# Kernel optimization log

Hardware: AMD Instinct MI355X
Metric: run time of the kernel (lower is better)

The kernel has to match this reference:

```python
import jax, jax.numpy as jnp
import numpy as np

NU, NI, D, H = 200000, 100000, 128, 128
E = 600000

def _segment_mean(vals, seg_ids, num_segments):
    s = jax.ops.segment_sum(vals, seg_ids, num_segments=num_segments)
    cnt = jax.ops.segment_sum(jnp.ones((vals.shape[0],), vals.dtype), seg_ids, num_segments=num_segments)
    return s / jnp.maximum(cnt, 1.0)[:, None]


def setup_inputs() -> dict:
    key = jax.random.key(0)
    ks = jax.random.split(key, 16)
    sc = 1.0 / np.sqrt(D)
    return {
        'x_user': jax.random.normal(ks[0], (NU, D), jnp.float32),
        'x_item': jax.random.normal(ks[1], (NI, D), jnp.float32),
        'edge_src_ui': jax.random.randint(ks[2], (E,), 0, NU),
        'edge_dst_ui': jax.random.randint(ks[3], (E,), 0, NI),
        'edge_src_iu': jax.random.randint(ks[4], (E,), 0, NI),
        'edge_dst_iu': jax.random.randint(ks[5], (E,), 0, NU),
        'Wl_ui': jax.random.normal(ks[6], (D, H), jnp.float32) * sc,
        'bl_ui': jax.random.normal(ks[7], (H,), jnp.float32) * 0.01,
        'Wr_ui': jax.random.normal(ks[8], (D, H), jnp.float32) * sc,
        'Wl_iu': jax.random.normal(ks[9], (D, H), jnp.float32) * sc,
        'bl_iu': jax.random.normal(ks[10], (H,), jnp.float32) * 0.01,
        'Wr_iu': jax.random.normal(ks[11], (D, H), jnp.float32) * sc,
        'W_user': jax.random.normal(ks[12], (H, H), jnp.float32) * sc,
        'b_user': jax.random.normal(ks[13], (H,), jnp.float32) * 0.01,
        'W_item': jax.random.normal(ks[14], (H, H), jnp.float32) * sc,
        'b_item': jax.random.normal(ks[15], (H,), jnp.float32) * 0.01,
    }


def reference(x_user, x_item, edge_src_ui, edge_dst_ui, edge_src_iu, edge_dst_iu,
              Wl_ui, bl_ui, Wr_ui, Wl_iu, bl_iu, Wr_iu,
              W_user, b_user, W_item, b_item):
    # SAGEConv per edge type: out_dst = mean_aggr(x_src[src]) @ Wl + bl + x_dst @ Wr
    agg_item = _segment_mean(x_user[edge_src_ui], edge_dst_ui, NI)   # [NI, D]
    h_item = agg_item @ Wl_ui + bl_ui + x_item @ Wr_ui               # [NI, H]
    agg_user = _segment_mean(x_item[edge_src_iu], edge_dst_iu, NU)   # [NU, D]
    h_user = agg_user @ Wl_iu + bl_iu + x_user @ Wr_iu               # [NU, H]
    # HeteroConv aggr='sum' is trivial here (one edge type per dst node type).
    out_user = jax.nn.relu(h_user @ W_user + b_user)
    out_item = jax.nn.relu(h_item @ W_item + b_item)
    return jnp.concatenate([out_user, out_item], axis=0)  # [NU+NI, H]
```

## Files before the change

### kernel.cpp

```cpp
#include <hip/hip_runtime.h>

#define NUu 200000
#define NIi 100000
#define EE  600000

#define SCAP 1024

typedef short short8 __attribute__((ext_vector_type(8)));
typedef float floatx4 __attribute__((ext_vector_type(4)));

__device__ __forceinline__ unsigned short f2bf(float f) {
  union { float f; unsigned int u; } v; v.f = f;
  unsigned int r = v.u + 0x7FFFu + ((v.u >> 16) & 1u);
  return (unsigned short)(r >> 16);
}

__global__ __launch_bounds__(128) void fuse_weights(
    const float* __restrict__ Wl_iu, const float* __restrict__ Wr_iu,
    const float* __restrict__ Wl_ui, const float* __restrict__ Wr_ui,
    const float* __restrict__ W_user, const float* __restrict__ W_item,
    unsigned short* __restrict__ Wp_user, unsigned short* __restrict__ Wp_item)
{
  int d = blockIdx.x;
  int m = blockIdx.y;
  int h = threadIdx.x;
  const float* A; const float* W; unsigned short* dst; int koff;
  switch (m) {
    case 0:  A = Wl_iu; W = W_user; dst = Wp_user; koff = 0;   break;
    case 1:  A = Wr_iu; W = W_user; dst = Wp_user; koff = 128; break;
    case 2:  A = Wl_ui; W = W_item; dst = Wp_item; koff = 0;   break;
    default: A = Wr_ui; W = W_item; dst = Wp_item; koff = 128; break;
  }
  float acc = 0.f;
  for (int k = 0; k < 128; ++k) acc += A[d * 128 + k] * W[k * 128 + h];
  int kg = koff + d;
  int ks = kg >> 5, quad = (kg >> 3) & 3, j = kg & 7;
  int nt = h >> 4, nlo = h & 15;
  int idx = ((nt * 8 + ks) * 64 + quad * 16 + nlo) * 8 + j;
  dst[idx] = f2bf(acc);
}

__global__ __launch_bounds__(128) void fuse_bias(
    const float* __restrict__ bl_iu, const float* __restrict__ b_user, const float* __restrict__ Wu,
    const float* __restrict__ bl_ui, const float* __restrict__ b_item, const float* __restrict__ Wi,
    float* __restrict__ bias_user, float* __restrict__ bias_item)
{
  int h = threadIdx.x;
  const float* bl = blockIdx.x ? bl_ui : bl_iu;
  const float* b2 = blockIdx.x ? b_item : b_user;
  const float* W  = blockIdx.x ? Wi : Wu;
  float* o        = blockIdx.x ? bias_item : bias_user;
  float acc = b2[h];
  for (int k = 0; k < 128; ++k) acc += bl[k] * W[k * 128 + h];
  o[h] = acc;
}

__global__ __launch_bounds__(256) void hist(const int* __restrict__ edst,
                                            int* __restrict__ cnt, int E)
{
  int e = blockIdx.x * 256 + threadIdx.x;
  if (e < E) atomicAdd(&cnt[edst[e]], 1);
}

__global__ __launch_bounds__(256) void scan1(const int* __restrict__ cnt,
                                             int* __restrict__ blksum, int N)
{
  __shared__ int s[256];
  int b = blockIdx.x, t = threadIdx.x;
  int base = b * 1024 + t * 4;
  int v = 0;
  #pragma unroll
  for (int j = 0; j < 4; ++j) { int i = base + j; if (i < N) v += cnt[i]; }
  s[t] = v; __syncthreads();
  for (int off = 128; off > 0; off >>= 1) {
    if (t < off) s[t] += s[t + off];
    __syncthreads();
  }
  if (t == 0) blksum[b] = s[0];
}

__global__ __launch_bounds__(256) void scan2(const int* __restrict__ blksum,
                                             int* __restrict__ blkoff, int nblk)
{
  __shared__ int s[256];
  int t = threadIdx.x;
  int v = t < nblk ? blksum[t] : 0;
  s[t] = v; __syncthreads();
  for (int off = 1; off < 256; off <<= 1) {
    int tmp = t >= off ? s[t - off] : 0;
    __syncthreads();
    s[t] += tmp;
    __syncthreads();
  }
  if (t < nblk) blkoff[t] = s[t] - v;
}

__global__ __launch_bounds__(256) void scan3(const int* __restrict__ cnt,
                                             const int* __restrict__ blkoff,
                                             int* __restrict__ rowp,
                                             int* __restrict__ fillp, int N)
{
  __shared__ int s[256];
  int b = blockIdx.x, t = threadIdx.x;
  int base = b * 1024 + t * 4;
  int v[4]; int sum = 0;
  #pragma unroll
  for (int j = 0; j < 4; ++j) { int i = base + j; v[j] = (i < N) ? cnt[i] : 0; sum += v[j]; }
  s[t] = sum; __syncthreads();
  for (int off = 1; off < 256; off <<= 1) {
    int tmp = t >= off ? s[t - off] : 0;
    __syncthreads();
    s[t] += tmp;
    __syncthreads();
  }
  int ex = s[t] - sum + blkoff[b];
  #pragma unroll
  for (int j = 0; j < 4; ++j) {
    int i = base + j;
    if (i < N) { rowp[i] = ex; fillp[i] = ex; ex += v[j]; }
  }
}

__global__ __launch_bounds__(256) void fill(const int* __restrict__ esrc,
                                            const int* __restrict__ edst,
                                            int* __restrict__ fillp,
                                            int* __restrict__ srcs, int E)
{
  int e = blockIdx.x * 256 + threadIdx.x;
  if (e < E) {
    int d = edst[e];
    int p = atomicAdd(&fillp[d], 1);
    srcs[p] = esrc[e];
  }
}

__global__ __launch_bounds__(256, 4) void fused_gemm(
    const float* __restrict__ xown, const float* __restrict__ xsrc,
    const int* __restrict__ rowp, const int* __restrict__ srcs,
    const unsigned short* __restrict__ Wp, const float* __restrict__ bias,
    float* __restrict__ outbase, int nvalid, int etotal)
{
  __shared__ __align__(16) uint4 ldsA4[2048];
  __shared__ int ldsS[SCAP];
  __shared__ int rb[65];
  int t = threadIdx.x;
  int node0 = blockIdx.x * 64;

  if (t < 65) {
    int node = node0 + t;
    rb[t] = node < nvalid ? rowp[node] : etotal;
  }
  __syncthreads();
  int rs0 = rb[0];
  int W = rb[64] - rs0;
  for (int idx = t; idx < W && idx < SCAP; idx += 256)
    ldsS[idx] = srcs[rs0 + idx];
  __syncthreads();

  #pragma unroll
  for (int i = 0; i < 8; ++i) {
    int oid = t + i * 256;
    int m = oid >> 5;
    int oct = oid & 31;
    int node = node0 + m;
    float vals[8];
    #pragma unroll
    for (int j2 = 0; j2 < 8; ++j2) vals[j2] = 0.f;
    if (node < nvalid) {
      if (oct < 16) {
        int k0 = oct * 8;
        int erel = rb[m] - rs0;
        int deg = rb[m + 1] - rb[m];
        float a0=0,a1=0,a2=0,a3=0,a4=0,a5=0,a6=0,a7=0;
        int e = 0;
        for (; e + 4 <= deg; e += 4) {
          int q0 = erel + e;
          int s0 = (q0+0 < SCAP) ? ldsS[q0+0] : srcs[rs0+q0+0];
          int s1 = (q0+1 < SCAP) ? ldsS[q0+1] : srcs[rs0+q0+1];
          int s2 = (q0+2 < SCAP) ? ldsS[q0+2] : srcs[rs0+q0+2];
          int s3 = (q0+3 < SCAP) ? ldsS[q0+3] : srcs[rs0+q0+3];
          const float4* r0 = (const float4*)(xsrc + (size_t)s0 * 128 + k0);
          const float4* r1 = (const float4*)(xsrc + (size_t)s1 * 128 + k0);
          const float4* r2 = (const float4*)(xsrc + (size_t)s2 * 128 + k0);
          const float4* r3 = (const float4*)(xsrc + (size_t)s3 * 128 + k0);
          float4 l0 = r0[0], h0 = r0[1];
          float4 l1 = r1[0], h1 = r1[1];
          float4 l2 = r2[0], h2 = r2[1];
          float4 l3 = r3[0], h3 = r3[1];
          a0 += l0.x + l1.x + l2.x + l3.x;
          a1 += l0.y + l1.y + l2.y + l3.y;
          a2 += l0.z + l1.z + l2.z + l3.z;
          a3 += l0.w + l1.w + l2.w + l3.w;
          a4 += h0.x + h1.x + h2.x + h3.x;
          a5 += h0.y + h1.y + h2.y + h3.y;
          a6 += h0.z + h1.z + h2.z + h3.z;
          a7 += h0.w + h1.w + h2.w + h3.w;
        }
        for (; e < deg; ++e) {
          int q = erel + e;
          int s = (q < SCAP) ? ldsS[q] : srcs[rs0 + q];
          const float4* r = (const float4*)(xsrc + (size_t)s * 128 + k0);
          float4 l = r[0], h = r[1];
          a0 += l.x; a1 += l.y; a2 += l.z; a3 += l.w;
          a4 += h.x; a5 += h.y; a6 += h.z; a7 += h.w;
        }
        float sc = deg > 0 ? 1.0f / (float)deg : 0.f;
        vals[0]=a0*sc; vals[1]=a1*sc; vals[2]=a2*sc; vals[3]=a3*sc;
        vals[4]=a4*sc; vals[5]=a5*sc; vals[6]=a6*sc; vals[7]=a7*sc;
      } else {
        int k0 = (oct - 16) * 8;
        const float4* p4 = (const float4*)(xown + (size_t)node * 128 + k0);
        float4 lo = p4[0], hi = p4[1];
        vals[0]=lo.x; vals[1]=lo.y; vals[2]=lo.z; vals[3]=lo.w;
        vals[4]=hi.x; vals[5]=hi.y; vals[6]=hi.z; vals[7]=hi.w;
      }
    }
    uint4 p;
    p.x = (unsigned)f2bf(vals[0]) | ((unsigned)f2bf(vals[1]) << 16);
    p.y = (unsigned)f2bf(vals[2]) | ((unsigned)f2bf(vals[3]) << 16);
    p.z = (unsigned)f2bf(vals[4]) | ((unsigned)f2bf(vals[5]) << 16);
    p.w = (unsigned)f2bf(vals[6]) | ((unsigned)f2bf(vals[7]) << 16);
    int ks = oct >> 2, quad = oct & 3;
    int mt = m >> 4, mlo = m & 15;
    ldsA4[(mt * 8 + ks) * 64 + quad * 16 + mlo] = p;
  }
  __syncthreads();

  int wave = t >> 6, lane = t & 63;
  floatx4 acc[8];
  #pragma unroll
  for (int i = 0; i < 8; ++i) acc[i] = (floatx4){0.f, 0.f, 0.f, 0.f};
  const short8* A = (const short8*)ldsA4;
  const short8* B = (const short8*)Wp;
  #pragma unroll
  for (int kk = 0; kk < 8; ++kk) {
    short8 af = A[(wave * 8 + kk) * 64 + lane];
    #pragma unroll
    for (int nt = 0; nt < 8; ++nt) {
      short8 bf = B[(nt * 8 + kk) * 64 + lane];
      acc[nt] = __builtin_amdgcn_mfma_f32_16x16x32_bf16(af, bf, acc[nt], 0, 0, 0);
    }
  }

  int col = lane & 15, qrow = (lane >> 4) * 4;
  #pragma unroll
  for (int nt = 0; nt < 8; ++nt) {
    int n = nt * 16 + col;
    float bv = bias[n];
    #pragma unroll
    for (int r2 = 0; r2 < 4; ++r2) {
      int node = node0 + wave * 16 + qrow + r2;
      if (node < nvalid) {
        float v = acc[nt][r2] + bv;
        outbase[(size_t)node * 128 + n] = v > 0.f ? v : 0.f;
      }
    }
  }
}

extern "C" void kernel_launch(void* const* d_in, const int* in_sizes, int n_in,
                              void* d_out, int out_size, void* d_ws, size_t ws_size,
                              hipStream_t stream)
{
  const float* x_user = (const float*)d_in[0];
  const float* x_item = (const float*)d_in[1];
  const int* esrc_ui  = (const int*)d_in[2];
  const int* edst_ui  = (const int*)d_in[3];
  const int* esrc_iu  = (const int*)d_in[4];
  const int* edst_iu  = (const int*)d_in[5];
  const float* Wl_ui  = (const float*)d_in[6];
  const float* bl_ui  = (const float*)d_in[7];
  const float* Wr_ui  = (const float*)d_in[8];
  const float* Wl_iu  = (const float*)d_in[9];
  const float* bl_iu  = (const float*)d_in[10];
  const float* Wr_iu  = (const float*)d_in[11];
  const float* W_user = (const float*)d_in[12];
  const float* b_user = (const float*)d_in[13];
  const float* W_item = (const float*)d_in[14];
  const float* b_item = (const float*)d_in[15];
  float* out = (float*)d_out;

  char* ws = (char*)d_ws;
  int* cnt_user  = (int*)(ws + 0);
  int* cnt_item  = (int*)(ws + 800000);
  int* row_user  = (int*)(ws + 1200000);
  int* row_item  = (int*)(ws + 2000000);
  int* fill_user = (int*)(ws + 2400000);
  int* fill_item = (int*)(ws + 3200000);
  int* srcs_user = (int*)(ws + 3600000);
  int* srcs_item = (int*)(ws + 6000000);
  int* blks_user = (int*)(ws + 8400000);
  int* blks_item = (int*)(ws + 8401024);
  int* boff_user = (int*)(ws + 8402048);
  int* boff_item = (int*)(ws + 8403072);
  unsigned short* Wp_user = (unsigned short*)(ws + 8404224);
  unsigned short* Wp_item = (unsigned short*)(ws + 8469760);
  float* bias_user = (float*)(ws + 8535296);
  float* bias_item = (float*)(ws + 8535808);

  hipMemsetAsync(d_ws, 0, 1200000, stream);

  fuse_weights<<<dim3(128, 4), 128, 0, stream>>>(Wl_iu, Wr_iu, Wl_ui, Wr_ui,
                                                 W_user, W_item, Wp_user, Wp_item);
  fuse_bias<<<2, 128, 0, stream>>>(bl_iu, b_user, W_user, bl_ui, b_item, W_item,
                                   bias_user, bias_item);

  const int EB = (EE + 255) / 256;
  const int NBU = (NUu + 1023) / 1024;
  const int NBI = (NIi + 1023) / 1024;

  hist<<<EB, 256, 0, stream>>>(edst_iu, cnt_user, EE);
  hist<<<EB, 256, 0, stream>>>(edst_ui, cnt_item, EE);

  scan1<<<NBU, 256, 0, stream>>>(cnt_user, blks_user, NUu);
  scan1<<<NBI, 256, 0, stream>>>(cnt_item, blks_item, NIi);
  scan2<<<1, 256, 0, stream>>>(blks_user, boff_user, NBU);
  scan2<<<1, 256, 0, stream>>>(blks_item, boff_item, NBI);
  scan3<<<NBU, 256, 0, stream>>>(cnt_user, boff_user, row_user, fill_user, NUu);
  scan3<<<NBI, 256, 0, stream>>>(cnt_item, boff_item, row_item, fill_item, NIi);

  fill<<<EB, 256, 0, stream>>>(esrc_iu, edst_iu, fill_user, srcs_user, EE);
  fill<<<EB, 256, 0, stream>>>(esrc_ui, edst_ui, fill_item, srcs_item, EE);

  fused_gemm<<<(NUu + 63) / 64, 256, 0, stream>>>(x_user, x_item, row_user,
                                                  srcs_user, Wp_user, bias_user,
                                                  out, NUu, EE);
  fused_gemm<<<(NIi + 63) / 64, 256, 0, stream>>>(x_item, x_user, row_item,
                                                  srcs_item, Wp_item, bias_item,
                                                  out + (size_t)NUu * 128, NIi, EE);
}
```

Baseline: 604.6 us.

## Merge user/item launches and split fused GEMM into two K-halves with swizzled LDS

```diff
diff --git a/kernel.cpp b/kernel.cpp
--- a/kernel.cpp
+++ b/kernel.cpp
@@ -5,6 +5,8 @@
 #define EE  600000
 
 #define SCAP 1024
+#define NB_USER 3125
+#define NB_ITEM 1563
 
 typedef short short8 __attribute__((ext_vector_type(8)));
 typedef float floatx4 __attribute__((ext_vector_type(4)));
@@ -55,18 +57,26 @@
   o[h] = acc;
 }
 
-__global__ __launch_bounds__(256) void hist(const int* __restrict__ edst,
-                                            int* __restrict__ cnt, int E)
+__global__ __launch_bounds__(256) void hist2(
+    const int* __restrict__ edst_iu, int* __restrict__ cnt_user,
+    const int* __restrict__ edst_ui, int* __restrict__ cnt_item)
 {
   int e = blockIdx.x * 256 + threadIdx.x;
-  if (e < E) atomicAdd(&cnt[edst[e]], 1);
-}
-
-__global__ __launch_bounds__(256) void scan1(const int* __restrict__ cnt,
-                                             int* __restrict__ blksum, int N)
+  if (e >= EE) return;
+  const int* edst = blockIdx.y ? edst_ui : edst_iu;
+  int* cnt        = blockIdx.y ? cnt_item : cnt_user;
+  atomicAdd(&cnt[edst[e]], 1);
+}
+
+__global__ __launch_bounds__(256) void scan1(
+    const int* __restrict__ cnt_u, int* __restrict__ blk_u,
+    const int* __restrict__ cnt_i, int* __restrict__ blk_i)
 {
   __shared__ int s[256];
   int b = blockIdx.x, t = threadIdx.x;
+  const int* cnt; int* blksum; int N;
+  if (blockIdx.y == 0) { cnt = cnt_u; blksum = blk_u; N = NUu; }
+  else { if (b >= 98) return; cnt = cnt_i; blksum = blk_i; N = NIi; }
   int base = b * 1024 + t * 4;
   int v = 0;
   #pragma unroll
@@ -79,11 +89,15 @@
   if (t == 0) blksum[b] = s[0];
 }
 
-__global__ __launch_bounds__(256) void scan2(const int* __restrict__ blksum,
-                                             int* __restrict__ blkoff, int nblk)
+__global__ __launch_bounds__(256) void scan2(
+    const int* __restrict__ bs_u, int* __restrict__ bo_u,
+    const int* __restrict__ bs_i, int* __restrict__ bo_i)
 {
   __shared__ int s[256];
   int t = threadIdx.x;
+  const int* blksum = blockIdx.x ? bs_i : bs_u;
+  int* blkoff       = blockIdx.x ? bo_i : bo_u;
+  int nblk          = blockIdx.x ? 98 : 196;
   int v = t < nblk ? blksum[t] : 0;
   s[t] = v; __syncthreads();
   for (int off = 1; off < 256; off <<= 1) {
@@ -95,13 +109,17 @@
   if (t < nblk) blkoff[t] = s[t] - v;
 }
 
-__global__ __launch_bounds__(256) void scan3(const int* __restrict__ cnt,
-                                             const int* __restrict__ blkoff,
-                                             int* __restrict__ rowp,
-                                             int* __restrict__ fillp, int N)
+__global__ __launch_bounds__(256) void scan3(
+    const int* __restrict__ cnt_u, const int* __restrict__ bo_u,
+    int* __restrict__ row_u, int* __restrict__ fil_u,
+    const int* __restrict__ cnt_i, const int* __restrict__ bo_i,
+    int* __restrict__ row_i, int* __restrict__ fil_i)
 {
   __shared__ int s[256];
   int b = blockIdx.x, t = threadIdx.x;
+  const int* cnt; const int* blkoff; int* rowp; int* fillp; int N;
+  if (blockIdx.y == 0) { cnt = cnt_u; blkoff = bo_u; rowp = row_u; fillp = fil_u; N = NUu; }
+  else { if (b >= 98) return; cnt = cnt_i; blkoff = bo_i; rowp = row_i; fillp = fil_i; N = NIi; }
   int base = b * 1024 + t * 4;
   int v[4]; int sum = 0;
   #pragma unroll
@@ -121,40 +139,95 @@
   }
 }
 
-__global__ __launch_bounds__(256) void fill(const int* __restrict__ esrc,
-                                            const int* __restrict__ edst,
-                                            int* __restrict__ fillp,
-                                            int* __restrict__ srcs, int E)
+__global__ __launch_bounds__(256) void fill2(
+    const int* __restrict__ esrc_iu, const int* __restrict__ edst_iu,
+    int* __restrict__ fill_user, int* __restrict__ srcs_user,
+    const int* __restrict__ esrc_ui, const int* __restrict__ edst_ui,
+    int* __restrict__ fill_item, int* __restrict__ srcs_item)
 {
   int e = blockIdx.x * 256 + threadIdx.x;
-  if (e < E) {
-    int d = edst[e];
-    int p = atomicAdd(&fillp[d], 1);
-    srcs[p] = esrc[e];
-  }
-}
-
-__global__ __launch_bounds__(256, 4) void fused_gemm(
-    const float* __restrict__ xown, const float* __restrict__ xsrc,
-    const int* __restrict__ rowp, const int* __restrict__ srcs,
-    const unsigned short* __restrict__ Wp, const float* __restrict__ bias,
-    float* __restrict__ outbase, int nvalid, int etotal)
-{
-  __shared__ __align__(16) uint4 ldsA4[2048];
+  if (e >= EE) return;
+  const int* esrc; const int* edst; int* fillp; int* srcs;
+  if (blockIdx.y == 0) { esrc = esrc_iu; edst = edst_iu; fillp = fill_user; srcs = srcs_user; }
+  else                 { esrc = esrc_ui; edst = edst_ui; fillp = fill_item; srcs = srcs_item; }
+  int d = edst[e];
+  int p = atomicAdd(&fillp[d], 1);
+  srcs[p] = esrc[e];
+}
+
+__global__ __launch_bounds__(256, 6) void fused_gemm(
+    const float* __restrict__ xu_own, const float* __restrict__ xu_src,
+    const int* __restrict__ rowp_u, const int* __restrict__ srcs_u,
+    const unsigned short* __restrict__ Wp_u, const float* __restrict__ bias_u,
+    const float* __restrict__ xi_own, const float* __restrict__ xi_src,
+    const int* __restrict__ rowp_i, const int* __restrict__ srcs_i,
+    const unsigned short* __restrict__ Wp_i, const float* __restrict__ bias_i,
+    float* __restrict__ out)
+{
+  __shared__ __align__(16) uint4 ldsA4[1024];
   __shared__ int ldsS[SCAP];
   __shared__ int rb[65];
   int t = threadIdx.x;
-  int node0 = blockIdx.x * 64;
+  int b = blockIdx.x;
+
+  const float* xown; const float* xsrc; const int* rowp; const int* srcs;
+  const unsigned short* Wp; const float* bias; float* outbase; int nvalid; int node0;
+  if (b < NB_USER) {
+    xown = xu_own; xsrc = xu_src; rowp = rowp_u; srcs = srcs_u;
+    Wp = Wp_u; bias = bias_u; outbase = out; nvalid = NUu; node0 = b * 64;
+  } else {
+    xown = xi_own; xsrc = xi_src; rowp = rowp_i; srcs = srcs_i;
+    Wp = Wp_i; bias = bias_i; outbase = out + (size_t)NUu * 128;
+    nvalid = NIi; node0 = (b - NB_USER) * 64;
+  }
 
   if (t < 65) {
     int node = node0 + t;
-    rb[t] = node < nvalid ? rowp[node] : etotal;
+    rb[t] = node < nvalid ? rowp[node] : EE;
   }
   __syncthreads();
   int rs0 = rb[0];
   int W = rb[64] - rs0;
   for (int idx = t; idx < W && idx < SCAP; idx += 256)
     ldsS[idx] = srcs[rs0 + idx];
+
+  #pragma unroll
+  for (int i = 0; i < 4; ++i) {
+    int oid = t + i * 256;
+    int m = oid >> 4;
+    int oct = oid & 15;
+    int node = node0 + m;
+    uint4 p; p.x = 0u; p.y = 0u; p.z = 0u; p.w = 0u;
+    if (node < nvalid) {
+      const float4* p4 = (const float4*)(xown + (size_t)node * 128 + oct * 8);
+      float4 lo = p4[0], hi = p4[1];
+      p.x = (unsigned)f2bf(lo.x) | ((unsigned)f2bf(lo.y) << 16);
+      p.y = (unsigned)f2bf(lo.z) | ((unsigned)f2bf(lo.w) << 16);
+      p.z = (unsigned)f2bf(hi.x) | ((unsigned)f2bf(hi.y) << 16);
+      p.w = (unsigned)f2bf(hi.z) | ((unsigned)f2bf(hi.w) << 16);
+    }
+    int ks = oct >> 2, quad = oct & 3;
+    int mt = m >> 4, mlo = m & 15;
+    ldsA4[(mt * 4 + ks) * 64 + quad * 16 + (mlo ^ (oct & 7))] = p;
+  }
+  __syncthreads();
+
+  int wave = t >> 6, lane = t & 63;
+  int quadr = lane >> 4, mlor = lane & 15;
+  floatx4 acc[8];
+  #pragma unroll
+  for (int i = 0; i < 8; ++i) acc[i] = (floatx4){0.f, 0.f, 0.f, 0.f};
+  const short8* A = (const short8*)ldsA4;
+  const short8* B = (const short8*)Wp;
+  #pragma unroll
+  for (int kk = 0; kk < 4; ++kk) {
+    short8 af = A[(wave * 4 + kk) * 64 + quadr * 16 + (mlor ^ ((kk * 4 + quadr) & 7))];
+    #pragma unroll
+    for (int nt = 0; nt < 8; ++nt) {
+      short8 bf = B[(nt * 8 + 4 + kk) * 64 + lane];
+      acc[nt] = __builtin_amdgcn_mfma_f32_16x16x32_bf16(af, bf, acc[nt], 0, 0, 0);
+    }
+  }
   __syncthreads();
 
   #pragma unroll
@@ -162,79 +235,59 @@
     int oid = t + i * 256;
     int m = oid >> 5;
     int oct = oid & 31;
+    int slice = oct & 15;
+    int par = oct >> 4;
     int node = node0 + m;
-    float vals[8];
-    #pragma unroll
-    for (int j2 = 0; j2 < 8; ++j2) vals[j2] = 0.f;
+    float a0=0,a1=0,a2=0,a3=0,a4=0,a5=0,a6=0,a7=0;
+    int deg = 0;
     if (node < nvalid) {
-      if (oct < 16) {
-        int k0 = oct * 8;
-        int erel = rb[m] - rs0;
-        int deg = rb[m + 1] - rb[m];
-        float a0=0,a1=0,a2=0,a3=0,a4=0,a5=0,a6=0,a7=0;
-        int e = 0;
-        for (; e + 4 <= deg; e += 4) {
-          int q0 = erel + e;
-          int s0 = (q0+0 < SCAP) ? ldsS[q0+0] : srcs[rs0+q0+0];
-          int s1 = (q0+1 < SCAP) ? ldsS[q0+1] : srcs[rs0+q0+1];
-          int s2 = (q0+2 < SCAP) ? ldsS[q0+2] : srcs[rs0+q0+2];
-          int s3 = (q0+3 < SCAP) ? ldsS[q0+3] : srcs[rs0+q0+3];
-          const float4* r0 = (const float4*)(xsrc + (size_t)s0 * 128 + k0);
-          const float4* r1 = (const float4*)(xsrc + (size_t)s1 * 128 + k0);
-          const float4* r2 = (const float4*)(xsrc + (size_t)s2 * 128 + k0);
-          const float4* r3 = (const float4*)(xsrc + (size_t)s3 * 128 + k0);
-          float4 l0 = r0[0], h0 = r0[1];
-          float4 l1 = r1[0], h1 = r1[1];
-          float4 l2 = r2[0], h2 = r2[1];
-          float4 l3 = r3[0], h3 = r3[1];
-          a0 += l0.x + l1.x + l2.x + l3.x;
-          a1 += l0.y + l1.y + l2.y + l3.y;
-          a2 += l0.z + l1.z + l2.z + l3.z;
-          a3 += l0.w + l1.w + l2.w + l3.w;
-          a4 += h0.x + h1.x + h2.x + h3.x;
-          a5 += h0.y + h1.y + h2.y + h3.y;
-          a6 += h0.z + h1.z + h2.z + h3.z;
-          a7 += h0.w + h1.w + h2.w + h3.w;
-        }
-        for (; e < deg; ++e) {
-          int q = erel + e;
-          int s = (q < SCAP) ? ldsS[q] : srcs[rs0 + q];
-          const float4* r = (const float4*)(xsrc + (size_t)s * 128 + k0);
-          float4 l = r[0], h = r[1];
-          a0 += l.x; a1 += l.y; a2 += l.z; a3 += l.w;
-          a4 += h.x; a5 += h.y; a6 += h.z; a7 += h.w;
-        }
-        float sc = deg > 0 ? 1.0f / (float)deg : 0.f;
-        vals[0]=a0*sc; vals[1]=a1*sc; vals[2]=a2*sc; vals[3]=a3*sc;
-        vals[4]=a4*sc; vals[5]=a5*sc; vals[6]=a6*sc; vals[7]=a7*sc;
-      } else {
-        int k0 = (oct - 16) * 8;
-        const float4* p4 = (const float4*)(xown + (size_t)node * 128 + k0);
-        float4 lo = p4[0], hi = p4[1];
-        vals[0]=lo.x; vals[1]=lo.y; vals[2]=lo.z; vals[3]=lo.w;
-        vals[4]=hi.x; vals[5]=hi.y; vals[6]=hi.z; vals[7]=hi.w;
+      int erel = rb[m] - rs0;
+      deg = rb[m + 1] - rb[m];
+      int k0 = slice * 8;
+      int e = par;
+      for (; e + 2 < deg; e += 4) {
+        int q0 = erel + e, q1 = q0 + 2;
+        int s0 = (q0 < SCAP) ? ldsS[q0] : srcs[rs0 + q0];
+        int s1 = (q1 < SCAP) ? ldsS[q1] : srcs[rs0 + q1];
+        const float4* r0 = (const float4*)(xsrc + (size_t)s0 * 128 + k0);
+        const float4* r1 = (const float4*)(xsrc + (size_t)s1 * 128 + k0);
+        float4 l0 = r0[0], h0 = r0[1];
+        float4 l1 = r1[0], h1 = r1[1];
+        a0 += l0.x + l1.x; a1 += l0.y + l1.y;
+        a2 += l0.z + l1.z; a3 += l0.w + l1.w;
+        a4 += h0.x + h1.x; a5 += h0.y + h1.y;
+        a6 += h0.z + h1.z; a7 += h0.w + h1.w;
       }
-    }
-    uint4 p;
-    p.x = (unsigned)f2bf(vals[0]) | ((unsigned)f2bf(vals[1]) << 16);
-    p.y = (unsigned)f2bf(vals[2]) | ((unsigned)f2bf(vals[3]) << 16);
-    p.z = (unsigned)f2bf(vals[4]) | ((unsigned)f2bf(vals[5]) << 16);
-    p.w = (unsigned)f2bf(vals[6]) | ((unsigned)f2bf(vals[7]) << 16);
-    int ks = oct >> 2, quad = oct & 3;
-    int mt = m >> 4, mlo = m & 15;
-    ldsA4[(mt * 8 + ks) * 64 + quad * 16 + mlo] = p;
+      if (e < deg) {
+        int q = erel + e;
+        int s = (q < SCAP) ? ldsS[q] : srcs[rs0 + q];
+        const float4* r = (const float4*)(xsrc + (size_t)s * 128 + k0);
+        float4 l = r[0], h = r[1];
+        a0 += l.x; a1 += l.y; a2 += l.z; a3 += l.w;
+        a4 += h.x; a5 += h.y; a6 += h.z; a7 += h.w;
+      }
+    }
+    a0 += __shfl_xor(a0, 16); a1 += __shfl_xor(a1, 16);
+    a2 += __shfl_xor(a2, 16); a3 += __shfl_xor(a3, 16);
+    a4 += __shfl_xor(a4, 16); a5 += __shfl_xor(a5, 16);
+    a6 += __shfl_xor(a6, 16); a7 += __shfl_xor(a7, 16);
+    if (par == 0) {
+      float sc = deg > 0 ? 1.0f / (float)deg : 0.f;
+      uint4 p;
+      p.x = (unsigned)f2bf(a0 * sc) | ((unsigned)f2bf(a1 * sc) << 16);
+      p.y = (unsigned)f2bf(a2 * sc) | ((unsigned)f2bf(a3 * sc) << 16);
+      p.z = (unsigned)f2bf(a4 * sc) | ((unsigned)f2bf(a5 * sc) << 16);
+      p.w = (unsigned)f2bf(a6 * sc) | ((unsigned)f2bf(a7 * sc) << 16);
+      int ks = slice >> 2, quad = slice & 3;
+      int mt = m >> 4, mlo = m & 15;
+      ldsA4[(mt * 4 + ks) * 64 + quad * 16 + (mlo ^ (slice & 7))] = p;
+    }
   }
   __syncthreads();
 
-  int wave = t >> 6, lane = t & 63;
-  floatx4 acc[8];
-  #pragma unroll
-  for (int i = 0; i < 8; ++i) acc[i] = (floatx4){0.f, 0.f, 0.f, 0.f};
-  const short8* A = (const short8*)ldsA4;
-  const short8* B = (const short8*)Wp;
-  #pragma unroll
-  for (int kk = 0; kk < 8; ++kk) {
-    short8 af = A[(wave * 8 + kk) * 64 + lane];
+  #pragma unroll
+  for (int kk = 0; kk < 4; ++kk) {
+    short8 af = A[(wave * 4 + kk) * 64 + quadr * 16 + (mlor ^ ((kk * 4 + quadr) & 7))];
     #pragma unroll
     for (int nt = 0; nt < 8; ++nt) {
       short8 bf = B[(nt * 8 + kk) * 64 + lane];
@@ -307,25 +360,16 @@
 
   const int EB = (EE + 255) / 256;
   const int NBU = (NUu + 1023) / 1024;
-  const int NBI = (NIi + 1023) / 1024;
-
-  hist<<<EB, 256, 0, stream>>>(edst_iu, cnt_user, EE);
-  hist<<<EB, 256, 0, stream>>>(edst_ui, cnt_item, EE);
-
-  scan1<<<NBU, 256, 0, stream>>>(cnt_user, blks_user, NUu);
-  scan1<<<NBI, 256, 0, stream>>>(cnt_item, blks_item, NIi);
-  scan2<<<1, 256, 0, stream>>>(blks_user, boff_user, NBU);
-  scan2<<<1, 256, 0, stream>>>(blks_item, boff_item, NBI);
-  scan3<<<NBU, 256, 0, stream>>>(cnt_user, boff_user, row_user, fill_user, NUu);
-  scan3<<<NBI, 256, 0, stream>>>(cnt_item, boff_item, row_item, fill_item, NIi);
-
-  fill<<<EB, 256, 0, stream>>>(esrc_iu, edst_iu, fill_user, srcs_user, EE);
-  fill<<<EB, 256, 0, stream>>>(esrc_ui, edst_ui, fill_item, srcs_item, EE);
-
-  fused_gemm<<<(NUu + 63) / 64, 256, 0, stream>>>(x_user, x_item, row_user,
-                                                  srcs_user, Wp_user, bias_user,
-                                                  out, NUu, EE);
-  fused_gemm<<<(NIi + 63) / 64, 256, 0, stream>>>(x_item, x_user, row_item,
-                                                  srcs_item, Wp_item, bias_item,
-                                                  out + (size_t)NUu * 128, NIi, EE);
-}
+
+  hist2<<<dim3(EB, 2), 256, 0, stream>>>(edst_iu, cnt_user, edst_ui, cnt_item);
+  scan1<<<dim3(NBU, 2), 256, 0, stream>>>(cnt_user, blks_user, cnt_item, blks_item);
+  scan2<<<2, 256, 0, stream>>>(blks_user, boff_user, blks_item, boff_item);
+  scan3<<<dim3(NBU, 2), 256, 0, stream>>>(cnt_user, boff_user, row_user, fill_user,
+                                          cnt_item, boff_item, row_item, fill_item);
+  fill2<<<dim3(EB, 2), 256, 0, stream>>>(esrc_iu, edst_iu, fill_user, srcs_user,
+                                         esrc_ui, edst_ui, fill_item, srcs_item);
+
+  fused_gemm<<<NB_USER + NB_ITEM, 256, 0, stream>>>(
+      x_user, x_item, row_user, srcs_user, Wp_user, bias_user,
+      x_item, x_user, row_item, srcs_item, Wp_item, bias_item, out);
+}
```

New measurement: 578.5 us. 1.05x faster.
